# Kernel optimization log

Measured on AMD Instinct MI355X. Metric: run time of the kernel, lower is better.

## Reference

```python
import jax, jax.numpy as jnp
import numpy as np

B, IN, H = 4096, 1024, 1024
G = 5  # i, f, o, c_hat, s gates

def setup_inputs() -> dict:
    key = jax.random.key(0)
    ks = jax.random.split(key, 24)
    s_in = 1.0 / np.sqrt(IN)
    s_h = 1.0 / np.sqrt(H)
    s_cat = 1.0 / np.sqrt(IN + H)
    inp = {
        'x': jax.random.normal(ks[0], (B, IN), jnp.float32),
        'h_prev': jax.random.normal(ks[1], (B, H), jnp.float32),
        'c_prev': jax.random.normal(ks[2], (B, H), jnp.float32),
        'ssg_state': jax.random.normal(ks[3], (B, H), jnp.float32),
        # stacked gate weights, torch Linear convention y = x @ W.T + b
        'Wx': jax.random.uniform(ks[4], (G, H, IN), jnp.float32, -s_in, s_in),
        'bWx': jax.random.uniform(ks[5], (G, H), jnp.float32, -s_in, s_in),
        'Ux': jax.random.uniform(ks[6], (G, H, H), jnp.float32, -s_h, s_h),
        'bUx': jax.random.uniform(ks[7], (G, H), jnp.float32, -s_h, s_h),
        # alpha MLP: Linear(IN+H -> H), ReLU, Linear(H -> 1), Sigmoid
        'a1_w': jax.random.uniform(ks[8], (H, IN + H), jnp.float32, -s_cat, s_cat),
        'a1_b': jax.random.uniform(ks[9], (H,), jnp.float32, -s_cat, s_cat),
        'a2_w': jax.random.uniform(ks[10], (1, H), jnp.float32, -s_h, s_h),
        'a2_b': jax.random.uniform(ks[11], (1,), jnp.float32, -s_h, s_h),
        'r1_w': jax.random.uniform(ks[12], (H, H), jnp.float32, -s_h, s_h),
        'r1_b': jax.random.uniform(ks[13], (H,), jnp.float32, -s_h, s_h),
        'r2_w': jax.random.uniform(ks[14], (H, H), jnp.float32, -s_h, s_h),
        'r2_b': jax.random.uniform(ks[15], (H,), jnp.float32, -s_h, s_h),
        'r3_w': jax.random.uniform(ks[16], (H, H), jnp.float32, -s_h, s_h),
        'r3_b': jax.random.uniform(ks[17], (H,), jnp.float32, -s_h, s_h),
        'ssg_w': jax.random.uniform(ks[18], (H, H), jnp.float32, -s_h, s_h),
        'ssg_b': jax.random.uniform(ks[19], (H,), jnp.float32, -s_h, s_h),
    }
    return inp


def reference(x, h_prev, c_prev, ssg_state, Wx, bWx, Ux, bUx,
              a1_w, a1_b, a2_w, a2_b, r1_w, r1_b, r2_w, r2_b, r3_w, r3_b,
              ssg_w, ssg_b):
    # all 5 gate pre-activations in two batched GEMMs: [G, B, H]
    g = (jnp.einsum('bi,ghi->gbh', x, Wx) + bWx[:, None, :]
         + jnp.einsum('bh,gkh->gbk', h_prev, Ux) + bUx[:, None, :])
    i_t = jax.nn.sigmoid(g[0])
    f_t = jax.nn.sigmoid(g[1])
    o_t = jax.nn.sigmoid(g[2])
    c_hat_t = jnp.tanh(g[3])
    s_t = jax.nn.sigmoid(g[4])  # computed as in original (unused when ssg_state given)

    combined = jnp.concatenate([x, h_prev], axis=-1)  # [B, IN+H]
    a_hidden = jax.nn.relu(combined @ a1_w.T + a1_b)
    alpha_t = jax.nn.sigmoid(a_hidden @ a2_w.T + a2_b)  # [B, 1]

    ssg_new = (ssg_state + h_prev) @ ssg_w.T + ssg_b  # ssg_state is not None branch

    c_t = f_t * c_prev + i_t * c_hat_t * s_t * alpha_t * ssg_new

    r = jax.nn.relu(h_prev @ r1_w.T + r1_b)
    r = jax.nn.relu(r @ r2_w.T + r2_b)
    residual = r @ r3_w.T + r3_b

    c_t = c_t + residual
    h_t = o_t * jnp.tanh(c_t)
    return (h_t, c_t, ssg_new)
```

## Files before the change

### kernel.cpp

```cpp
#include <hip/hip_runtime.h>
#include <hip/hip_bf16.h>

#define B_DIM 4096
#define H_DIM 1024
#define K1    2048
#define N1    6144
#define N2    2048
#define NT1   (K1 / 64)

typedef __attribute__((ext_vector_type(8))) short bf16x8;
typedef __attribute__((ext_vector_type(4))) float f32x4;

__device__ __forceinline__ unsigned short f2bf(float f) {
  unsigned int x = __float_as_uint(f);
  x += 0x7fffu + ((x >> 16) & 1u);
  return (unsigned short)(x >> 16);
}
__device__ __forceinline__ float bf2f(unsigned short u) {
  return __uint_as_float(((unsigned int)u) << 16);
}
__device__ __forceinline__ float fast_sigmoid(float x) {
  return __builtin_amdgcn_rcpf(1.0f + __expf(-x));
}
__device__ __forceinline__ float fast_tanh(float x) {
  return 1.0f - 2.0f * __builtin_amdgcn_rcpf(1.0f + __expf(2.0f * x));
}
__device__ __forceinline__ void gload_lds16(const void* g, void* l) {
  __builtin_amdgcn_global_load_lds(
      (const __attribute__((address_space(1))) void*)g,
      (__attribute__((address_space(3))) void*)l, 16, 0, 0);
}

__device__ __forceinline__ int swz1k(int x) {
  return x ^ (((x >> 9) & 1) << 5);
}

__global__ __launch_bounds__(256) void prep_kernel(
    const float* __restrict__ x, const float* __restrict__ h,
    const float* __restrict__ ssg_state,
    const float* __restrict__ Wx, const float* __restrict__ Ux,
    const float* __restrict__ a1_w,
    const float* __restrict__ ssg_w, const float* __restrict__ r1_w,
    const float* __restrict__ r2_w, const float* __restrict__ r3_w,
    unsigned short* __restrict__ combined,
    unsigned short* __restrict__ ssg_in,
    unsigned short* __restrict__ hprev_bf,
    unsigned short* __restrict__ W1,
    unsigned short* __restrict__ W2,
    unsigned short* __restrict__ W3,
    unsigned short* __restrict__ W4)
{
  const size_t NV0 = (size_t)B_DIM * K1 / 4;
  const size_t NV1 = (size_t)B_DIM * H_DIM / 4;
  const size_t NV2 = NV1;
  const size_t NV3 = (size_t)N1 * K1 / 4;
  const size_t NV4 = (size_t)N2 * H_DIM / 4;
  const size_t NV5 = (size_t)H_DIM * H_DIM / 4;
  const size_t total = NV0 + NV1 + NV2 + NV3 + NV4 + NV5 + NV5;
  const size_t stride = (size_t)gridDim.x * blockDim.x;

  for (size_t v = (size_t)blockIdx.x * blockDim.x + threadIdx.x; v < total; v += stride) {
    size_t idx = v;
    const float* src;
    unsigned short* dst;
    if (idx < NV0) {
      size_t e = idx * 4, b = e >> 11, k = e & 2047;
      src = (k < 1024) ? &x[(b << 10) + k] : &h[(b << 10) + (k - 1024)];
      dst = &combined[e];
    } else if ((idx -= NV0) < NV1) {
      size_t e = idx * 4;
      float4 a = *(const float4*)&ssg_state[e];
      float4 c = *(const float4*)&h[e];
      ushort4 o;
      o.x = f2bf(a.x + c.x); o.y = f2bf(a.y + c.y);
      o.z = f2bf(a.z + c.z); o.w = f2bf(a.w + c.w);
      *(ushort4*)&ssg_in[e] = o;
      continue;
    } else if ((idx -= NV1) < NV2) {
      size_t e = idx * 4; src = &h[e]; dst = &hprev_bf[e];
    } else if ((idx -= NV2) < NV3) {
      size_t e = idx * 4, n = e >> 11, k = e & 2047;
      if (n < 5120) src = (k < 1024) ? &Wx[(n << 10) + k] : &Ux[(n << 10) + (k - 1024)];
      else          src = &a1_w[((n - 5120) << 11) + k];
      dst = &W1[e];
    } else if ((idx -= NV3) < NV4) {
      size_t e = idx * 4, n = e >> 10, k = e & 1023;
      src = (n < 1024) ? &ssg_w[(n << 10) + k] : &r1_w[((n - 1024) << 10) + k];
      dst = &W2[e];
    } else if ((idx -= NV4) < NV5) {
      size_t e = idx * 4; src = &r2_w[e]; dst = &W3[e];
    } else {
      idx -= NV5;
      size_t e = idx * 4; src = &r3_w[e]; dst = &W4[e];
    }
    float4 a = *(const float4*)src;
    ushort4 o;
    o.x = f2bf(a.x); o.y = f2bf(a.y); o.z = f2bf(a.z); o.w = f2bf(a.w);
    *(ushort4*)dst = o;
  }
}

__global__ __launch_bounds__(512, 2) void gemm8p_mode0(
    const unsigned short* __restrict__ A,
    const unsigned short* __restrict__ W,
    const float* __restrict__ bWx, const float* __restrict__ bUx,
    const float* __restrict__ a1_b,
    unsigned short* __restrict__ gates,
    unsigned short* __restrict__ a_hidden)
{
  __shared__ unsigned short lds[49152];

  const int tid  = threadIdx.x;
  const int wave = tid >> 6;
  const int lane = tid & 63;
  const int wm = wave >> 2;
  const int wn = wave & 3;

  const int NWG = (B_DIM / 128) * (N1 / 256);
  const int swz = (blockIdx.x & 7) * (NWG / 8) + (blockIdx.x >> 3);
  const int ntn = N1 / 256;
  const int tm = swz / ntn, tn = swz % ntn;
  const int tmB = tm * 128, tnB = tn * 256;

  const int sidx = swz1k(lane * 16);
  const int r_l  = sidx >> 6;
  const int kel  = (sidx & 63) >> 1;
  const unsigned short* pA[2];
  const unsigned short* pB[2];
#pragma unroll
  for (int j = 0; j < 2; ++j) {
    const int rr = wave * 16 + r_l;
    const int kk0 = j * 32 + kel;
    pA[j] = A + (size_t)(tmB + rr) * K1 + kk0;
    pB[j] = W + (size_t)(tnB + rr) * K1 + kk0;
  }

#define STAGE_A(tt) do { const int p_ = (tt) & 1;                                \
    gload_lds16(pA[0] + (size_t)(tt) * 64,                                       \
                &lds[p_ * 24576 + (wave * 2 + 0) * 512]);                        \
    gload_lds16(pA[1] + (size_t)(tt) * 64,                                       \
                &lds[p_ * 24576 + (wave * 2 + 1) * 512]); } while (0)
#define STAGE_B(tt, h_) do { const int p_ = (tt) & 1;                            \
    gload_lds16(pB[0] + (size_t)(h_) * 128 * K1 + (tt) * 64,                     \
                &lds[p_ * 24576 + 8192 + (h_) * 8192 + (wave * 2 + 0) * 512]);   \
    gload_lds16(pB[1] + (size_t)(h_) * 128 * K1 + (tt) * 64,                     \
                &lds[p_ * 24576 + 8192 + (h_) * 8192 + (wave * 2 + 1) * 512]); } while (0)

  const int loc = swz1k((lane & 15) * 64 + (lane >> 4) * 16);

  f32x4 acc[4][4];
#pragma unroll
  for (int m = 0; m < 4; ++m)
#pragma unroll
    for (int n = 0; n < 4; ++n) acc[m][n] = (f32x4){0.f, 0.f, 0.f, 0.f};

  STAGE_A(0); STAGE_B(0, 0); STAGE_B(0, 1);

#define MFMA16(aV, bV) do {                                                      \
    _Pragma("unroll")                                                            \
    for (int n = 0; n < 4; ++n) {                                                \
      _Pragma("unroll")                                                          \
      for (int m = 0; m < 4; ++m)                                                \
        acc[m][n] = __builtin_amdgcn_mfma_f32_16x16x32_bf16(                     \
            aV[m], bV[n], acc[m][n], 0, 0, 0);                                   \
    } } while (0)

  const char* lchar = (const char*)lds;
  for (int t = 0; t < NT1; ++t) {
    asm volatile("s_waitcnt vmcnt(0)" ::: "memory");
    __builtin_amdgcn_s_barrier();

    const char* base = lchar + (t & 1) * 49152;
    const char* bA = base + wm * 8192 + loc;
    const char* bB = base + 16384 + wn * 8192 + loc;

    bf16x8 a0[4], a1[4], b0[4], b1[4];
#pragma unroll
    for (int n = 0; n < 4; ++n) b0[n] = *(const bf16x8*)(bB + (2 * n + 0) * 1024);
#pragma unroll
    for (int m = 0; m < 4; ++m) a0[m] = *(const bf16x8*)(bA + (2 * m + 0) * 1024);
    if (t + 1 < NT1) STAGE_A(t + 1);
#pragma unroll
    for (int n = 0; n < 4; ++n) b1[n] = *(const bf16x8*)(bB + (2 * n + 1) * 1024);
#pragma unroll
    for (int m = 0; m < 4; ++m) a1[m] = *(const bf16x8*)(bA + (2 * m + 1) * 1024);
    if (t + 1 < NT1) { STAGE_B(t + 1, 0); STAGE_B(t + 1, 1); }

    __builtin_amdgcn_s_setprio(1);
    MFMA16(a0, b0);
    __builtin_amdgcn_s_setprio(0);
    __builtin_amdgcn_s_setprio(1);
    MFMA16(a1, b1);
    __builtin_amdgcn_s_setprio(0);
  }
#undef MFMA16
#undef STAGE_A
#undef STAGE_B

  unsigned short* slab = &lds[wave * 1024];
  const int l15 = lane & 15, lq4 = (lane >> 4) << 2;
  const int lr8 = lane >> 3, lc8 = lane & 7;
  const bool isgate = (tn < 20);
  const int g = tn >> 2;
  const int colg0 = (isgate ? (tn & 3) : (tn - 20)) * 256 + wn * 64;
  unsigned short* outbase = isgate ? (gates + (size_t)g * ((size_t)B_DIM * 1024))
                                   : a_hidden;
  const int rowg0 = tmB + wm * 64;
  float biasv[4];
#pragma unroll
  for (int fn = 0; fn < 4; ++fn) {
    const int c = colg0 + fn * 16 + l15;
    biasv[fn] = isgate ? (bWx[g * 1024 + c] + bUx[g * 1024 + c]) : a1_b[c];
  }
  __builtin_amdgcn_s_barrier();
#pragma unroll
  for (int fm = 0; fm < 4; ++fm) {
#pragma unroll
    for (int fn = 0; fn < 4; ++fn) {
      f32x4 v = acc[fm][fn];
#pragma unroll
      for (int j = 0; j < 4; ++j) {
        const int row = lq4 + j;
        const float xv = v[j] + biasv[fn];
        const float res = isgate ? ((g == 3) ? fast_tanh(xv) : fast_sigmoid(xv))
                                 : fmaxf(xv, 0.f);
        const int colb = ((fn * 16 + l15) * 2) ^ (((row >> 2) & 3) << 5);
        slab[(row * 128 + colb) >> 1] = f2bf(res);
      }
    }
    asm volatile("s_waitcnt lgkmcnt(0)" ::: "memory");
    __builtin_amdgcn_sched_barrier(0);
#pragma unroll
    for (int rd = 0; rd < 2; ++rd) {
      const int row = rd * 8 + lr8;
      const int cb = (lc8 * 16) ^ (((row >> 2) & 3) << 5);
      bf16x8 pk = *(const bf16x8*)((const char*)slab + row * 128 + cb);
      const size_t r = (size_t)(rowg0 + fm * 16 + row);
      *(bf16x8*)&outbase[r * 1024 + colg0 + lc8 * 8] = pk;
    }
    asm volatile("s_waitcnt lgkmcnt(0)" ::: "memory");
    __builtin_amdgcn_sched_barrier(0);
  }
}

template <int MODE>
__global__ __launch_bounds__(256, 3) void gemm_bf16(
    const unsigned short* __restrict__ A0g,
    const unsigned short* __restrict__ A1g,
    const unsigned short* __restrict__ Wg,
    const int M, const int N, const int K,
    const float* __restrict__ b0, const float* __restrict__ b1,
    void* __restrict__ out0, void* __restrict__ out1)
{
  __shared__ unsigned short As[128 * 64];
  __shared__ unsigned short Bs[128 * 64];

  const int tid  = threadIdx.x;
  const int wave = tid >> 6;
  const int lane = tid & 63;
  const int wm = wave >> 1, wn = wave & 1;

  const int ntn = N >> 7;
  const int tm = blockIdx.x / ntn;
  const int tn = blockIdx.x % ntn;

  const unsigned short* Ag = A0g;
  if (MODE == 1 && tn >= 8) Ag = A1g;

  const int lrow = lane >> 3;
  const int lk   = (lane & 7) * 8;
  size_t a_off[4], b_off[4];
#pragma unroll
  for (int i = 0; i < 4; ++i) {
    int c = wave * 4 + i;
    int row = c * 8 + lrow;
    a_off[i] = (size_t)(tm * 128 + row) * K + lk;
    b_off[i] = (size_t)(tn * 128 + row) * K + lk;
  }

  f32x4 acc[4][4];
#pragma unroll
  for (int m = 0; m < 4; ++m)
#pragma unroll
    for (int n = 0; n < 4; ++n) acc[m][n] = (f32x4){0.f, 0.f, 0.f, 0.f};

  const int arow  = wm * 64 + (lane & 15);
  const int brow  = wn * 64 + (lane & 15);
  const int kfrag = (lane >> 4) * 8;

  for (int k0 = 0; k0 < K; k0 += 64) {
#pragma unroll
    for (int i = 0; i < 4; ++i) {
      gload_lds16(Ag + a_off[i] + k0, &As[(wave * 4 + i) * 512]);
      gload_lds16(Wg + b_off[i] + k0, &Bs[(wave * 4 + i) * 512]);
    }
    __syncthreads();
#pragma unroll
    for (int kk = 0; kk < 2; ++kk) {
      bf16x8 af[4], bfr[4];
#pragma unroll
      for (int m = 0; m < 4; ++m)
        af[m] = *(const bf16x8*)&As[(arow + m * 16) * 64 + kk * 32 + kfrag];
#pragma unroll
      for (int n = 0; n < 4; ++n)
        bfr[n] = *(const bf16x8*)&Bs[(brow + n * 16) * 64 + kk * 32 + kfrag];
#pragma unroll
      for (int m = 0; m < 4; ++m)
#pragma unroll
        for (int n = 0; n < 4; ++n)
          acc[m][n] = __builtin_amdgcn_mfma_f32_16x16x32_bf16(
              af[m], bfr[n], acc[m][n], 0, 0, 0);
    }
    __syncthreads();
  }

  const int col0 = tn * 128 + wn * 64;
  const int row0 = tm * 128 + wm * 64 + ((lane >> 4) << 2);
#pragma unroll
  for (int n = 0; n < 4; ++n) {
    const int col = col0 + n * 16 + (lane & 15);
    float bias;
    if (MODE == 1)      bias = (col < 1024) ? b0[col] : b1[col - 1024];
    else                bias = b0[col];
#pragma unroll
    for (int m = 0; m < 4; ++m) {
      const int rowb = row0 + m * 16;
      f32x4 v = acc[m][n];
#pragma unroll
      for (int j = 0; j < 4; ++j) {
        const float xv = v[j] + bias;
        const int r = rowb + j;
        if (MODE == 1) {
          if (col < 1024) {
            ((float*)out0)[(size_t)r * 1024 + col] = xv;
          } else {
            ((unsigned short*)out1)[(size_t)r * 1024 + (col - 1024)] = f2bf(fmaxf(xv, 0.f));
          }
        } else if (MODE == 2) {
          ((unsigned short*)out0)[(size_t)r * 1024 + col] = f2bf(fmaxf(xv, 0.f));
        } else {
          ((float*)out0)[(size_t)r * 1024 + col] = xv;
        }
      }
    }
  }
}

__global__ __launch_bounds__(256) void alpha_kernel(
    const unsigned short* __restrict__ a_hidden,
    const float* __restrict__ a2_w, const float* __restrict__ a2_b,
    float* __restrict__ alpha)
{
  const int wave = threadIdx.x >> 6, lane = threadIdx.x & 63;
  const int row = blockIdx.x * 4 + wave;
  const unsigned short* ah = a_hidden + (size_t)row * 1024;
  float sum = 0.f;
#pragma unroll
  for (int half = 0; half < 2; ++half) {
    const int h0 = half * 512 + lane * 8;
    ushort4 u0 = *(const ushort4*)&ah[h0];
    ushort4 u1 = *(const ushort4*)&ah[h0 + 4];
    float4 w0 = *(const float4*)&a2_w[h0];
    float4 w1 = *(const float4*)&a2_w[h0 + 4];
    sum += bf2f(u0.x) * w0.x + bf2f(u0.y) * w0.y + bf2f(u0.z) * w0.z + bf2f(u0.w) * w0.w;
    sum += bf2f(u1.x) * w1.x + bf2f(u1.y) * w1.y + bf2f(u1.z) * w1.z + bf2f(u1.w) * w1.w;
  }
#pragma unroll
  for (int off = 32; off; off >>= 1) sum += __shfl_xor(sum, off);
  if (lane == 0) alpha[row] = fast_sigmoid(sum + a2_b[0]);
}

__global__ __launch_bounds__(256) void final_elem_kernel(
    const unsigned short* __restrict__ gates,
    const float* __restrict__ c_prev,
    const float* __restrict__ alpha,
    const float* __restrict__ residual,
    const float* __restrict__ ssg_new,
    float* __restrict__ h_out, float* __restrict__ c_out)
{
  const size_t BH = (size_t)B_DIM * H_DIM;
  const size_t e = ((size_t)blockIdx.x * blockDim.x + threadIdx.x) * 4;
  if (e >= BH) return;
  const float al = alpha[e >> 10];
  ushort4 iu = *(const ushort4*)&gates[e];
  ushort4 fu = *(const ushort4*)&gates[BH + e];
  ushort4 ou = *(const ushort4*)&gates[2 * BH + e];
  ushort4 cu = *(const ushort4*)&gates[3 * BH + e];
  ushort4 su = *(const ushort4*)&gates[4 * BH + e];
  float4 cp = *(const float4*)&c_prev[e];
  float4 rs = *(const float4*)&residual[e];
  float4 sg = *(const float4*)&ssg_new[e];
  float4 ho, co;
  co.x = bf2f(fu.x) * cp.x + bf2f(iu.x) * bf2f(cu.x) * bf2f(su.x) * al * sg.x + rs.x;
  co.y = bf2f(fu.y) * cp.y + bf2f(iu.y) * bf2f(cu.y) * bf2f(su.y) * al * sg.y + rs.y;
  co.z = bf2f(fu.z) * cp.z + bf2f(iu.z) * bf2f(cu.z) * bf2f(su.z) * al * sg.z + rs.z;
  co.w = bf2f(fu.w) * cp.w + bf2f(iu.w) * bf2f(cu.w) * bf2f(su.w) * al * sg.w + rs.w;
  ho.x = bf2f(ou.x) * fast_tanh(co.x);
  ho.y = bf2f(ou.y) * fast_tanh(co.y);
  ho.z = bf2f(ou.z) * fast_tanh(co.z);
  ho.w = bf2f(ou.w) * fast_tanh(co.w);
  *(float4*)&h_out[e] = ho;
  *(float4*)&c_out[e] = co;
}

extern "C" void kernel_launch(void* const* d_in, const int* in_sizes, int n_in,
                              void* d_out, int out_size, void* d_ws, size_t ws_size,
                              hipStream_t stream)
{
  (void)in_sizes; (void)n_in; (void)out_size; (void)ws_size;
  const float* x         = (const float*)d_in[0];
  const float* h_prev    = (const float*)d_in[1];
  const float* c_prev    = (const float*)d_in[2];
  const float* ssg_state = (const float*)d_in[3];
  const float* Wx        = (const float*)d_in[4];
  const float* bWx       = (const float*)d_in[5];
  const float* Ux        = (const float*)d_in[6];
  const float* bUx       = (const float*)d_in[7];
  const float* a1_w      = (const float*)d_in[8];
  const float* a1_b      = (const float*)d_in[9];
  const float* a2_w      = (const float*)d_in[10];
  const float* a2_b      = (const float*)d_in[11];
  const float* r1_w      = (const float*)d_in[12];
  const float* r1_b      = (const float*)d_in[13];
  const float* r2_w      = (const float*)d_in[14];
  const float* r2_b      = (const float*)d_in[15];
  const float* r3_w      = (const float*)d_in[16];
  const float* r3_b      = (const float*)d_in[17];
  const float* ssg_w     = (const float*)d_in[18];
  const float* ssg_b     = (const float*)d_in[19];

  char* ws = (char*)d_ws;
  unsigned short* combined = (unsigned short*)(ws);
  unsigned short* ssg_in   = (unsigned short*)(ws + 16777216);
  unsigned short* hprev_bf = (unsigned short*)(ws + 25165824);
  unsigned short* W1       = (unsigned short*)(ws + 33554432);
  unsigned short* W2       = (unsigned short*)(ws + 58720256);
  unsigned short* W3       = (unsigned short*)(ws + 62914560);
  unsigned short* W4       = (unsigned short*)(ws + 65011712);
  unsigned short* gates    = (unsigned short*)(ws + 67108864);
  unsigned short* a_hidden = (unsigned short*)(ws + 109051904);
  float*          alpha    = (float*)(ws + 117440512);
  unsigned short* r1       = (unsigned short*)(ws + 117456896);
  unsigned short* r2       = (unsigned short*)(ws + 125845504);
  float*          residual = (float*)(ws + 134234112);

  float* h_out   = (float*)d_out;
  float* c_out   = h_out + (size_t)B_DIM * H_DIM;
  float* ssg_out = c_out + (size_t)B_DIM * H_DIM;

  prep_kernel<<<4096, 256, 0, stream>>>(x, h_prev, ssg_state, Wx, Ux, a1_w,
                                        ssg_w, r1_w, r2_w, r3_w,
                                        combined, ssg_in, hprev_bf, W1, W2, W3, W4);

  gemm8p_mode0<<<(B_DIM / 128) * (N1 / 256), 512, 0, stream>>>(
      combined, W1, bWx, bUx, a1_b, gates, a_hidden);

  gemm_bf16<1><<<(B_DIM / 128) * (N2 / 128), 256, 0, stream>>>(
      ssg_in, hprev_bf, W2, B_DIM, N2, 1024, ssg_b, r1_b, ssg_out, r1);

  gemm_bf16<2><<<(B_DIM / 128) * (1024 / 128), 256, 0, stream>>>(
      r1, r1, W3, B_DIM, 1024, 1024, r2_b, nullptr, r2, nullptr);

  gemm_bf16<3><<<(B_DIM / 128) * (1024 / 128), 256, 0, stream>>>(
      r2, r2, W4, B_DIM, 1024, 1024, r3_b, nullptr, residual, nullptr);

  alpha_kernel<<<B_DIM / 4, 256, 0, stream>>>(a_hidden, a2_w, a2_b, alpha);

  final_elem_kernel<<<(B_DIM * H_DIM / 4) / 256, 256, 0, stream>>>(
      gates, c_prev, alpha, residual, ssg_out, h_out, c_out);
}
```

Before: 269.8 us.

## Generalize pipelined GEMM to 128x128 tiles, reuse combined buffer, fuse alpha into final

The 512-thread 128x256 gate GEMM becomes a templated 256-thread 128x128 kernel with double-buffered LDS. The same kernel now also runs the ssg/r1 GEMM, whose h_prev operand is read straight from the combined buffer with stride 2048, so the separate hprev_bf conversion pass goes away. The alpha reduction is folded into the final elementwise kernel, one block per row, which removes a launch and the alpha buffer. Smaller tiles mean more workgroups and less reuse per tile, in exchange for better occupancy and less prep traffic.

Measured after the change: 247.9 us. -8.1%, faster.

```diff
diff --git a/kernel.cpp b/kernel.cpp
--- a/kernel.cpp
+++ b/kernel.cpp
@@ -5,8 +5,6 @@
 #define H_DIM 1024
 #define K1    2048
 #define N1    6144
-#define N2    2048
-#define NT1   (K1 / 64)
 
 typedef __attribute__((ext_vector_type(8))) short bf16x8;
 typedef __attribute__((ext_vector_type(4))) float f32x4;
@@ -44,7 +42,6 @@
     const float* __restrict__ r2_w, const float* __restrict__ r3_w,
     unsigned short* __restrict__ combined,
     unsigned short* __restrict__ ssg_in,
-    unsigned short* __restrict__ hprev_bf,
     unsigned short* __restrict__ W1,
     unsigned short* __restrict__ W2,
     unsigned short* __restrict__ W3,
@@ -52,11 +49,10 @@
 {
   const size_t NV0 = (size_t)B_DIM * K1 / 4;
   const size_t NV1 = (size_t)B_DIM * H_DIM / 4;
-  const size_t NV2 = NV1;
   const size_t NV3 = (size_t)N1 * K1 / 4;
-  const size_t NV4 = (size_t)N2 * H_DIM / 4;
+  const size_t NV4 = (size_t)2048 * H_DIM / 4;
   const size_t NV5 = (size_t)H_DIM * H_DIM / 4;
-  const size_t total = NV0 + NV1 + NV2 + NV3 + NV4 + NV5 + NV5;
+  const size_t total = NV0 + NV1 + NV3 + NV4 + NV5 + NV5;
   const size_t stride = (size_t)gridDim.x * blockDim.x;
 
   for (size_t v = (size_t)blockIdx.x * blockDim.x + threadIdx.x; v < total; v += stride) {
@@ -76,9 +72,7 @@
       o.z = f2bf(a.z + c.z); o.w = f2bf(a.w + c.w);
       *(ushort4*)&ssg_in[e] = o;
       continue;
-    } else if ((idx -= NV1) < NV2) {
-      size_t e = idx * 4; src = &h[e]; dst = &hprev_bf[e];
-    } else if ((idx -= NV2) < NV3) {
+    } else if ((idx -= NV1) < NV3) {
       size_t e = idx * 4, n = e >> 11, k = e & 2047;
       if (n < 5120) src = (k < 1024) ? &Wx[(n << 10) + k] : &Ux[(n << 10) + (k - 1024)];
       else          src = &a1_w[((n - 5120) << 11) + k];
@@ -100,51 +94,67 @@
   }
 }
 
-__global__ __launch_bounds__(512, 2) void gemm8p_mode0(
-    const unsigned short* __restrict__ A,
+template <int NT, int MODE>
+__global__ __launch_bounds__(256, 2) void gemm_fr(
+    const unsigned short* __restrict__ A0,
+    const unsigned short* __restrict__ A1,
     const unsigned short* __restrict__ W,
-    const float* __restrict__ bWx, const float* __restrict__ bUx,
-    const float* __restrict__ a1_b,
-    unsigned short* __restrict__ gates,
-    unsigned short* __restrict__ a_hidden)
+    const float* __restrict__ b0, const float* __restrict__ b1,
+    const float* __restrict__ b2,
+    void* __restrict__ out0, void* __restrict__ out1)
 {
-  __shared__ unsigned short lds[49152];
+  __shared__ unsigned short lds[32768];
+
+  constexpr int KDIM = NT * 64;
+  constexpr int N    = (MODE == 0) ? N1 : 2048;
+  constexpr int NTN  = N / 128;
+  constexpr int NWG  = (B_DIM / 128) * NTN;
 
   const int tid  = threadIdx.x;
   const int wave = tid >> 6;
   const int lane = tid & 63;
-  const int wm = wave >> 2;
-  const int wn = wave & 3;
-
-  const int NWG = (B_DIM / 128) * (N1 / 256);
+  const int wm = wave >> 1;
+  const int wn = wave & 1;
+
   const int swz = (blockIdx.x & 7) * (NWG / 8) + (blockIdx.x >> 3);
-  const int ntn = N1 / 256;
-  const int tm = swz / ntn, tn = swz % ntn;
-  const int tmB = tm * 128, tnB = tn * 256;
+  const int tm = swz / NTN, tn = swz % NTN;
+  const int tmB = tm * 128, tnB = tn * 128;
+
+  const unsigned short* Abase = A0;
+  int lda = (MODE == 0) ? K1 : 1024;
+  if (MODE == 1 && tn >= 8) { Abase = A1; lda = 2048; }
 
   const int sidx = swz1k(lane * 16);
   const int r_l  = sidx >> 6;
   const int kel  = (sidx & 63) >> 1;
-  const unsigned short* pA[2];
-  const unsigned short* pB[2];
-#pragma unroll
-  for (int j = 0; j < 2; ++j) {
-    const int rr = wave * 16 + r_l;
-    const int kk0 = j * 32 + kel;
-    pA[j] = A + (size_t)(tmB + rr) * K1 + kk0;
-    pB[j] = W + (size_t)(tnB + rr) * K1 + kk0;
-  }
+  const unsigned short* pA[2][2];
+  const unsigned short* pB[2][2];
+#pragma unroll
+  for (int rg = 0; rg < 2; ++rg)
+#pragma unroll
+    for (int j = 0; j < 2; ++j) {
+      const int rr = wave * 32 + rg * 16 + r_l;
+      const int kk0 = j * 32 + kel;
+      pA[rg][j] = Abase + (size_t)(tmB + rr) * lda + kk0;
+      pB[rg][j] = W + (size_t)(tnB + rr) * KDIM + kk0;
+    }
 
 #define STAGE_A(tt) do { const int p_ = (tt) & 1;                                \
-    gload_lds16(pA[0] + (size_t)(tt) * 64,                                       \
-                &lds[p_ * 24576 + (wave * 2 + 0) * 512]);                        \
-    gload_lds16(pA[1] + (size_t)(tt) * 64,                                       \
-                &lds[p_ * 24576 + (wave * 2 + 1) * 512]); } while (0)
-#define STAGE_B(tt, h_) do { const int p_ = (tt) & 1;                            \
-    gload_lds16(pB[0] + (size_t)(h_) * 128 * K1 + (tt) * 64,                     \
-                &lds[p_ * 24576 + 8192 + (h_) * 8192 + (wave * 2 + 0) * 512]);   \
-    gload_lds16(pB[1] + (size_t)(h_) * 128 * K1 + (tt) * 64,                     \
-                &lds[p_ * 24576 + 8192 + (h_) * 8192 + (wave * 2 + 1) * 512]); } while (0)
+    _Pragma("unroll")                                                            \
+    for (int rg = 0; rg < 2; ++rg)                                               \
+      _Pragma("unroll")                                                          \
+      for (int j = 0; j < 2; ++j)                                                \
+        gload_lds16(pA[rg][j] + (size_t)(tt) * 64,                               \
+                    &lds[p_ * 16384 + ((wave * 2 + rg) * 2 + j) * 512]);         \
+  } while (0)
+#define STAGE_B(tt) do { const int p_ = (tt) & 1;                                \
+    _Pragma("unroll")                                                            \
+    for (int rg = 0; rg < 2; ++rg)                                               \
+      _Pragma("unroll")                                                          \
+      for (int j = 0; j < 2; ++j)                                                \
+        gload_lds16(pB[rg][j] + (size_t)(tt) * 64,                               \
+                    &lds[p_ * 16384 + 8192 + ((wave * 2 + rg) * 2 + j) * 512]);  \
+  } while (0)
 
   const int loc = swz1k((lane & 15) * 64 + (lane >> 4) * 16);
 
@@ -154,7 +164,7 @@
 #pragma unroll
     for (int n = 0; n < 4; ++n) acc[m][n] = (f32x4){0.f, 0.f, 0.f, 0.f};
 
-  STAGE_A(0); STAGE_B(0, 0); STAGE_B(0, 1);
+  STAGE_A(0); STAGE_B(0);
 
 #define MFMA16(aV, bV) do {                                                      \
     _Pragma("unroll")                                                            \
@@ -166,11 +176,11 @@
     } } while (0)
 
   const char* lchar = (const char*)lds;
-  for (int t = 0; t < NT1; ++t) {
+  for (int t = 0; t < NT; ++t) {
     asm volatile("s_waitcnt vmcnt(0)" ::: "memory");
     __builtin_amdgcn_s_barrier();
 
-    const char* base = lchar + (t & 1) * 49152;
+    const char* base = lchar + (t & 1) * 32768;
     const char* bA = base + wm * 8192 + loc;
     const char* bB = base + 16384 + wn * 8192 + loc;
 
@@ -179,12 +189,12 @@
     for (int n = 0; n < 4; ++n) b0[n] = *(const bf16x8*)(bB + (2 * n + 0) * 1024);
 #pragma unroll
     for (int m = 0; m < 4; ++m) a0[m] = *(const bf16x8*)(bA + (2 * m + 0) * 1024);
-    if (t + 1 < NT1) STAGE_A(t + 1);
+    if (t + 1 < NT) STAGE_A(t + 1);
 #pragma unroll
     for (int n = 0; n < 4; ++n) b1[n] = *(const bf16x8*)(bB + (2 * n + 1) * 1024);
 #pragma unroll
     for (int m = 0; m < 4; ++m) a1[m] = *(const bf16x8*)(bA + (2 * m + 1) * 1024);
-    if (t + 1 < NT1) { STAGE_B(t + 1, 0); STAGE_B(t + 1, 1); }
+    if (t + 1 < NT) STAGE_B(t + 1);
 
     __builtin_amdgcn_s_setprio(1);
     MFMA16(a0, b0);
@@ -197,20 +207,50 @@
 #undef STAGE_A
 #undef STAGE_B
 
+  const int l15 = lane & 15, lq4 = (lane >> 4) << 2;
+  const int rowg0 = tmB + wm * 64;
+
+  if (MODE == 1 && tn < 8) {
+    const int col0 = tn * 128 + wn * 64;
+#pragma unroll
+    for (int fn = 0; fn < 4; ++fn) {
+      const int col = col0 + fn * 16 + l15;
+      const float bias = b0[col];
+#pragma unroll
+      for (int fm = 0; fm < 4; ++fm) {
+        f32x4 v = acc[fm][fn];
+#pragma unroll
+        for (int j = 0; j < 4; ++j) {
+          const int r = rowg0 + fm * 16 + lq4 + j;
+          ((float*)out0)[(size_t)r * 1024 + col] = v[j] + bias;
+        }
+      }
+    }
+    return;
+  }
+
   unsigned short* slab = &lds[wave * 1024];
-  const int l15 = lane & 15, lq4 = (lane >> 4) << 2;
   const int lr8 = lane >> 3, lc8 = lane & 7;
-  const bool isgate = (tn < 20);
-  const int g = tn >> 2;
-  const int colg0 = (isgate ? (tn & 3) : (tn - 20)) * 256 + wn * 64;
-  unsigned short* outbase = isgate ? (gates + (size_t)g * ((size_t)B_DIM * 1024))
-                                   : a_hidden;
-  const int rowg0 = tmB + wm * 64;
+  bool isgate = false;
+  int g = 0, colg0, rowplane = 0;
+  unsigned short* outbase;
+  if (MODE == 0) {
+    isgate = (tn < 40);
+    g = tn >> 3;
+    colg0 = (isgate ? (tn & 7) : (tn - 40)) * 128 + wn * 64;
+    outbase = isgate ? ((unsigned short*)out0 + (size_t)g * ((size_t)B_DIM * 1024))
+                     : (unsigned short*)out1;
+    (void)rowplane;
+  } else {
+    colg0 = (tn - 8) * 128 + wn * 64;
+    outbase = (unsigned short*)out1;
+  }
   float biasv[4];
 #pragma unroll
   for (int fn = 0; fn < 4; ++fn) {
     const int c = colg0 + fn * 16 + l15;
-    biasv[fn] = isgate ? (bWx[g * 1024 + c] + bUx[g * 1024 + c]) : a1_b[c];
+    if (MODE == 0) biasv[fn] = isgate ? (b0[g * 1024 + c] + b1[g * 1024 + c]) : b2[c];
+    else           biasv[fn] = b1[c];
   }
   __builtin_amdgcn_s_barrier();
 #pragma unroll
@@ -222,8 +262,9 @@
       for (int j = 0; j < 4; ++j) {
         const int row = lq4 + j;
         const float xv = v[j] + biasv[fn];
-        const float res = isgate ? ((g == 3) ? fast_tanh(xv) : fast_sigmoid(xv))
-                                 : fmaxf(xv, 0.f);
+        float res;
+        if (MODE == 0 && isgate) res = (g == 3) ? fast_tanh(xv) : fast_sigmoid(xv);
+        else                     res = fmaxf(xv, 0.f);
         const int colb = ((fn * 16 + l15) * 2) ^ (((row >> 2) & 3) << 5);
         slab[(row * 128 + colb) >> 1] = f2bf(res);
       }
@@ -246,11 +287,10 @@
 template <int MODE>
 __global__ __launch_bounds__(256, 3) void gemm_bf16(
     const unsigned short* __restrict__ A0g,
-    const unsigned short* __restrict__ A1g,
     const unsigned short* __restrict__ Wg,
     const int M, const int N, const int K,
-    const float* __restrict__ b0, const float* __restrict__ b1,
-    void* __restrict__ out0, void* __restrict__ out1)
+    const float* __restrict__ b0,
+    void* __restrict__ out0)
 {
   __shared__ unsigned short As[128 * 64];
   __shared__ unsigned short Bs[128 * 64];
@@ -263,9 +303,6 @@
   const int ntn = N >> 7;
   const int tm = blockIdx.x / ntn;
   const int tn = blockIdx.x % ntn;
-
-  const unsigned short* Ag = A0g;
-  if (MODE == 1 && tn >= 8) Ag = A1g;
 
   const int lrow = lane >> 3;
   const int lk   = (lane & 7) * 8;
@@ -291,7 +328,7 @@
   for (int k0 = 0; k0 < K; k0 += 64) {
 #pragma unroll
     for (int i = 0; i < 4; ++i) {
-      gload_lds16(Ag + a_off[i] + k0, &As[(wave * 4 + i) * 512]);
+      gload_lds16(A0g + a_off[i] + k0, &As[(wave * 4 + i) * 512]);
       gload_lds16(Wg + b_off[i] + k0, &Bs[(wave * 4 + i) * 512]);
     }
     __syncthreads();
@@ -319,9 +356,7 @@
 #pragma unroll
   for (int n = 0; n < 4; ++n) {
     const int col = col0 + n * 16 + (lane & 15);
-    float bias;
-    if (MODE == 1)      bias = (col < 1024) ? b0[col] : b1[col - 1024];
-    else                bias = b0[col];
+    const float bias = b0[col];
 #pragma unroll
     for (int m = 0; m < 4; ++m) {
       const int rowb = row0 + m * 16;
@@ -330,13 +365,7 @@
       for (int j = 0; j < 4; ++j) {
         const float xv = v[j] + bias;
         const int r = rowb + j;
-        if (MODE == 1) {
-          if (col < 1024) {
-            ((float*)out0)[(size_t)r * 1024 + col] = xv;
-          } else {
-            ((unsigned short*)out1)[(size_t)r * 1024 + (col - 1024)] = f2bf(fmaxf(xv, 0.f));
-          }
-        } else if (MODE == 2) {
+        if (MODE == 2) {
           ((unsigned short*)out0)[(size_t)r * 1024 + col] = f2bf(fmaxf(xv, 0.f));
         } else {
           ((float*)out0)[(size_t)r * 1024 + col] = xv;
@@ -346,42 +375,35 @@
   }
 }
 
-__global__ __launch_bounds__(256) void alpha_kernel(
+__global__ __launch_bounds__(256) void final_fused(
+    const unsigned short* __restrict__ gates,
+    const float* __restrict__ c_prev,
     const unsigned short* __restrict__ a_hidden,
     const float* __restrict__ a2_w, const float* __restrict__ a2_b,
-    float* __restrict__ alpha)
-{
-  const int wave = threadIdx.x >> 6, lane = threadIdx.x & 63;
-  const int row = blockIdx.x * 4 + wave;
-  const unsigned short* ah = a_hidden + (size_t)row * 1024;
-  float sum = 0.f;
-#pragma unroll
-  for (int half = 0; half < 2; ++half) {
-    const int h0 = half * 512 + lane * 8;
-    ushort4 u0 = *(const ushort4*)&ah[h0];
-    ushort4 u1 = *(const ushort4*)&ah[h0 + 4];
-    float4 w0 = *(const float4*)&a2_w[h0];
-    float4 w1 = *(const float4*)&a2_w[h0 + 4];
-    sum += bf2f(u0.x) * w0.x + bf2f(u0.y) * w0.y + bf2f(u0.z) * w0.z + bf2f(u0.w) * w0.w;
-    sum += bf2f(u1.x) * w1.x + bf2f(u1.y) * w1.y + bf2f(u1.z) * w1.z + bf2f(u1.w) * w1.w;
-  }
-#pragma unroll
-  for (int off = 32; off; off >>= 1) sum += __shfl_xor(sum, off);
-  if (lane == 0) alpha[row] = fast_sigmoid(sum + a2_b[0]);
-}
-
-__global__ __launch_bounds__(256) void final_elem_kernel(
-    const unsigned short* __restrict__ gates,
-    const float* __restrict__ c_prev,
-    const float* __restrict__ alpha,
     const float* __restrict__ residual,
     const float* __restrict__ ssg_new,
     float* __restrict__ h_out, float* __restrict__ c_out)
 {
+  __shared__ float red[5];
+  const int r = blockIdx.x;
+  const int tid = threadIdx.x;
   const size_t BH = (size_t)B_DIM * H_DIM;
-  const size_t e = ((size_t)blockIdx.x * blockDim.x + threadIdx.x) * 4;
-  if (e >= BH) return;
-  const float al = alpha[e >> 10];
+
+  {
+    ushort4 u = *(const ushort4*)&a_hidden[(size_t)r * 1024 + tid * 4];
+    float4 w = *(const float4*)&a2_w[tid * 4];
+    float s = bf2f(u.x) * w.x + bf2f(u.y) * w.y + bf2f(u.z) * w.z + bf2f(u.w) * w.w;
+#pragma unroll
+    for (int off = 32; off; off >>= 1) s += __shfl_xor(s, off);
+    if ((tid & 63) == 0) red[tid >> 6] = s;
+  }
+  __syncthreads();
+  if (tid == 0)
+    red[4] = fast_sigmoid(red[0] + red[1] + red[2] + red[3] + a2_b[0]);
+  __syncthreads();
+  const float al = red[4];
+
+  const size_t e = (size_t)r * 1024 + tid * 4;
   ushort4 iu = *(const ushort4*)&gates[e];
   ushort4 fu = *(const ushort4*)&gates[BH + e];
   ushort4 ou = *(const ushort4*)&gates[2 * BH + e];
@@ -432,14 +454,12 @@
   char* ws = (char*)d_ws;
   unsigned short* combined = (unsigned short*)(ws);
   unsigned short* ssg_in   = (unsigned short*)(ws + 16777216);
-  unsigned short* hprev_bf = (unsigned short*)(ws + 25165824);
   unsigned short* W1       = (unsigned short*)(ws + 33554432);
   unsigned short* W2       = (unsigned short*)(ws + 58720256);
   unsigned short* W3       = (unsigned short*)(ws + 62914560);
   unsigned short* W4       = (unsigned short*)(ws + 65011712);
   unsigned short* gates    = (unsigned short*)(ws + 67108864);
   unsigned short* a_hidden = (unsigned short*)(ws + 109051904);
-  float*          alpha    = (float*)(ws + 117440512);
   unsigned short* r1       = (unsigned short*)(ws + 117456896);
   unsigned short* r2       = (unsigned short*)(ws + 125845504);
   float*          residual = (float*)(ws + 134234112);
@@ -450,22 +470,20 @@
 
   prep_kernel<<<4096, 256, 0, stream>>>(x, h_prev, ssg_state, Wx, Ux, a1_w,
                                         ssg_w, r1_w, r2_w, r3_w,
-                                        combined, ssg_in, hprev_bf, W1, W2, W3, W4);
-
-  gemm8p_mode0<<<(B_DIM / 128) * (N1 / 256), 512, 0, stream>>>(
-      combined, W1, bWx, bUx, a1_b, gates, a_hidden);
-
-  gemm_bf16<1><<<(B_DIM / 128) * (N2 / 128), 256, 0, stream>>>(
-      ssg_in, hprev_bf, W2, B_DIM, N2, 1024, ssg_b, r1_b, ssg_out, r1);
+                                        combined, ssg_in, W1, W2, W3, W4);
+
+  gemm_fr<32, 0><<<(B_DIM / 128) * (N1 / 128), 256, 0, stream>>>(
+      combined, nullptr, W1, bWx, bUx, a1_b, gates, a_hidden);
+
+  gemm_fr<16, 1><<<(B_DIM / 128) * (2048 / 128), 256, 0, stream>>>(
+      ssg_in, combined + 1024, W2, ssg_b, r1_b, nullptr, ssg_out, r1);
 
   gemm_bf16<2><<<(B_DIM / 128) * (1024 / 128), 256, 0, stream>>>(
-      r1, r1, W3, B_DIM, 1024, 1024, r2_b, nullptr, r2, nullptr);
+      r1, W3, B_DIM, 1024, 1024, r2_b, r2);
 
   gemm_bf16<3><<<(B_DIM / 128) * (1024 / 128), 256, 0, stream>>>(
-      r2, r2, W4, B_DIM, 1024, 1024, r3_b, nullptr, residual, nullptr);
-
-  alpha_kernel<<<B_DIM / 4, 256, 0, stream>>>(a_hidden, a2_w, a2_b, alpha);
-
-  final_elem_kernel<<<(B_DIM * H_DIM / 4) / 256, 256, 0, stream>>>(
-      gates, c_prev, alpha, residual, ssg_out, h_out, c_out);
-}
+      r2, W4, B_DIM, 1024, 1024, r3_b, residual);
+
+  final_fused<<<B_DIM, 256, 0, stream>>>(
+      gates, c_prev, a_hidden, a2_w, a2_b, residual, ssg_out, h_out, c_out);
+}
```
